# Kernel optimization log

Measured on AMD Instinct MI355X. Metric: run time of the kernel, lower is better.

## Reference

```python
import jax, jax.numpy as jnp
import numpy as np

N = 8192        # nodes
F_IN = 512      # input feature dim
H1 = 256        # args.hidden1
H2 = 64         # args.hidden2
E = 262144      # edges (avg degree 32)


def setup_inputs() -> dict:
    key = jax.random.key(0)
    ks = jax.random.split(key, 7)
    x = jax.random.normal(ks[0], (N, F_IN), dtype=jnp.float32)
    adj_rows = jax.random.randint(ks[1], (E,), 0, N, dtype=jnp.int32)
    adj_cols = jax.random.randint(ks[2], (E,), 0, N, dtype=jnp.int32)
    adj_vals = jax.random.uniform(ks[3], (E,), dtype=jnp.float32)
    # Xavier-uniform init like reset_parameters()
    def xavier(k, fan_in, fan_out):
        lim = jnp.sqrt(6.0 / (fan_in + fan_out))
        return jax.random.uniform(k, (fan_in, fan_out), jnp.float32, -lim, lim)
    W1 = xavier(ks[4], F_IN, H1)
    W2 = xavier(ks[5], H1, H2)
    W3 = xavier(ks[6], H1, H2)
    return {"x": x, "adj_rows": adj_rows, "adj_cols": adj_cols,
            "adj_vals": adj_vals, "W1": W1, "W2": W2, "W3": W3}


def reference(x, adj_rows, adj_cols, adj_vals, W1, W2, W3):
    n = x.shape[0]

    def spmm(support):
        # sparse [N,N] @ dense [N,D]: gather neighbor rows, scale, scatter-add
        return jax.ops.segment_sum(adj_vals[:, None] * support[adj_cols],
                                   adj_rows, num_segments=n)

    # gc1: dropout(no-op, eval) -> x @ W1 -> SpMM -> relu
    h1 = jax.nn.relu(spmm(x @ W1))
    # gc2 / gc3: identity activation
    mu = spmm(h1 @ W2)
    logvar = spmm(h1 @ W3)
    z = mu  # eval-mode reparameterize returns mu
    # InnerProductDecoder with identity act (dropout no-op in eval)
    adj_recon = z @ z.T  # [N, N]
    return adj_recon, z, mu, logvar
```

## Files before the change

kernel.cpp:

```cpp
#include <hip/hip_runtime.h>
#include <hip/hip_bf16.h>

#define N_NODES 8192
#define F_INDIM 512
#define H1DIM   256
#define H2DIM   64

typedef __bf16 bf16x8 __attribute__((ext_vector_type(8)));
typedef float  floatx4 __attribute__((ext_vector_type(4)));

__global__ void count_rows(const int* __restrict__ rows, int* __restrict__ cnt, int e) {
    int i = blockIdx.x * blockDim.x + threadIdx.x;
    if (i < e) atomicAdd(&cnt[rows[i]], 1);
}

__global__ void scan_rows(const int* __restrict__ cnt, int* __restrict__ row_ptr,
                          int* __restrict__ cursor, int n) {
    __shared__ int sums[1024];
    int t = threadIdx.x;
    int base = t * 8;
    int loc[8];
    int s = 0;
#pragma unroll
    for (int i = 0; i < 8; ++i) { loc[i] = cnt[base + i]; s += loc[i]; }
    sums[t] = s;
    __syncthreads();
    for (int off = 1; off < 1024; off <<= 1) {
        int v = (t >= off) ? sums[t - off] : 0;
        __syncthreads();
        sums[t] += v;
        __syncthreads();
    }
    int run = sums[t] - s;
#pragma unroll
    for (int i = 0; i < 8; ++i) {
        row_ptr[base + i] = run;
        cursor[base + i]  = run;
        run += loc[i];
    }
    if (t == 1023) row_ptr[n] = run;
}

__global__ void scatter_edges(const int* __restrict__ rows, const int* __restrict__ cols,
                              const float* __restrict__ vals, int* __restrict__ cursor,
                              int* __restrict__ csr_col, float* __restrict__ csr_val, int e) {
    int i = blockIdx.x * blockDim.x + threadIdx.x;
    if (i < e) {
        int r = rows[i];
        int slot = atomicAdd(&cursor[r], 1);
        csr_col[slot] = cols[i];
        csr_val[slot] = vals[i];
    }
}

__global__ __launch_bounds__(256) void gemm1_f32(const float* __restrict__ A,
                                                 const float* __restrict__ B,
                                                 float* __restrict__ C) {
    constexpr int K = F_INDIM, NN = H1DIM;
    constexpr int BK = 16, LD = 68;
    __shared__ float As[BK][LD];
    __shared__ float Bs[BK][LD];
    const int tid = threadIdx.x;
    const int tx = tid & 15;
    const int ty = tid >> 4;
    const int bm = blockIdx.y * 64;
    const int bn = blockIdx.x * 64;
    float acc[4][4] = {};

    const int arow = tid >> 2, akc = (tid & 3) * 4;
    const int bkk = tid >> 4, bnc = (tid & 15) * 4;

    for (int k0 = 0; k0 < K; k0 += BK) {
        floatx4 av = *(const floatx4*)&A[(size_t)(bm + arow) * K + k0 + akc];
#pragma unroll
        for (int j = 0; j < 4; ++j) As[akc + j][arow] = av[j];
        *(floatx4*)&Bs[bkk][bnc] = *(const floatx4*)&B[(size_t)(k0 + bkk) * NN + bn + bnc];
        __syncthreads();
#pragma unroll
        for (int kk = 0; kk < BK; ++kk) {
            floatx4 a = *(const floatx4*)&As[kk][ty * 4];
            floatx4 b = *(const floatx4*)&Bs[kk][tx * 4];
#pragma unroll
            for (int i = 0; i < 4; ++i)
#pragma unroll
                for (int j = 0; j < 4; ++j) acc[i][j] += a[i] * b[j];
        }
        __syncthreads();
    }
#pragma unroll
    for (int i = 0; i < 4; ++i) {
        floatx4 o = {acc[i][0], acc[i][1], acc[i][2], acc[i][3]};
        *(floatx4*)&C[(size_t)(bm + ty * 4 + i) * NN + bn + tx * 4] = o;
    }
}

__global__ __launch_bounds__(256) void gemm23_f32(const float* __restrict__ A,
                                                  const float* __restrict__ W2,
                                                  const float* __restrict__ W3,
                                                  float* __restrict__ C2,
                                                  float* __restrict__ C3) {
    constexpr int K = H1DIM, NO = H2DIM;
    constexpr int BK = 16, LDA = 68, LDB = 136;
    __shared__ float As[BK][LDA];
    __shared__ float Bs[BK][LDB];
    const int tid = threadIdx.x;
    const int tx = tid & 15;
    const int ty = tid >> 4;
    const int bm = blockIdx.x * 64;
    float acc[4][8] = {};

    const int arow = tid >> 2, akc = (tid & 3) * 4;

    for (int k0 = 0; k0 < K; k0 += BK) {
        floatx4 av = *(const floatx4*)&A[(size_t)(bm + arow) * K + k0 + akc];
#pragma unroll
        for (int j = 0; j < 4; ++j) As[akc + j][arow] = av[j];
#pragma unroll
        for (int v = 0; v < 2; ++v) {
            int idx = tid + v * 256;
            int kk = idx >> 5, nc = (idx & 31) * 4;
            const float* src = (nc < 64) ? &W2[(size_t)(k0 + kk) * NO + nc]
                                         : &W3[(size_t)(k0 + kk) * NO + nc - 64];
            *(floatx4*)&Bs[kk][nc] = *(const floatx4*)src;
        }
        __syncthreads();
#pragma unroll
        for (int kk = 0; kk < BK; ++kk) {
            floatx4 a = *(const floatx4*)&As[kk][ty * 4];
            floatx4 b0 = *(const floatx4*)&Bs[kk][tx * 8];
            floatx4 b1 = *(const floatx4*)&Bs[kk][tx * 8 + 4];
#pragma unroll
            for (int i = 0; i < 4; ++i) {
#pragma unroll
                for (int j = 0; j < 4; ++j) acc[i][j] += a[i] * b0[j];
#pragma unroll
                for (int j = 0; j < 4; ++j) acc[i][j + 4] += a[i] * b1[j];
            }
        }
        __syncthreads();
    }
    const int c0 = tx * 8;
#pragma unroll
    for (int i = 0; i < 4; ++i) {
        floatx4 o0 = {acc[i][0], acc[i][1], acc[i][2], acc[i][3]};
        floatx4 o1 = {acc[i][4], acc[i][5], acc[i][6], acc[i][7]};
        size_t row = bm + ty * 4 + i;
        if (c0 < 64) {
            *(floatx4*)&C2[row * NO + c0] = o0;
            *(floatx4*)&C2[row * NO + c0 + 4] = o1;
        } else {
            *(floatx4*)&C3[row * NO + c0 - 64] = o0;
            *(floatx4*)&C3[row * NO + c0 - 60] = o1;
        }
    }
}

__global__ __launch_bounds__(256) void spmm_h1(const int* __restrict__ row_ptr,
                                               const int* __restrict__ csr_col,
                                               const float* __restrict__ csr_val,
                                               const float* __restrict__ in,
                                               float* __restrict__ out) {
    __shared__ int   s_col[256];
    __shared__ float s_val[256];
    const int r = blockIdx.x;
    const int d = threadIdx.x;
    const int beg = row_ptr[r];
    const int deg = row_ptr[r + 1] - beg;
    float acc = 0.f;
    for (int base = 0; base < deg; base += 256) {
        __syncthreads();
        if (base + d < deg) {
            s_col[d] = csr_col[beg + base + d];
            s_val[d] = csr_val[beg + base + d];
        }
        __syncthreads();
        int m = deg - base; if (m > 256) m = 256;
        int e = 0;
        for (; e + 4 <= m; e += 4) {
            float x0 = in[(size_t)s_col[e]     * H1DIM + d];
            float x1 = in[(size_t)s_col[e + 1] * H1DIM + d];
            float x2 = in[(size_t)s_col[e + 2] * H1DIM + d];
            float x3 = in[(size_t)s_col[e + 3] * H1DIM + d];
            acc += s_val[e] * x0 + s_val[e + 1] * x1 + s_val[e + 2] * x2 + s_val[e + 3] * x3;
        }
        for (; e < m; ++e) acc += s_val[e] * in[(size_t)s_col[e] * H1DIM + d];
    }
    out[(size_t)r * H1DIM + d] = fmaxf(acc, 0.f);
}

__global__ __launch_bounds__(256) void spmm_mu_logvar(const int* __restrict__ row_ptr,
                                                      const int* __restrict__ csr_col,
                                                      const float* __restrict__ csr_val,
                                                      const float* __restrict__ t2,
                                                      const float* __restrict__ t3,
                                                      float* __restrict__ mu,
                                                      float* __restrict__ z,
                                                      float* __restrict__ logvar,
                                                      __hip_bfloat16* __restrict__ zb) {
    __shared__ int   s_col[2][128];
    __shared__ float s_val[2][128];
    __shared__ int   s_deg[2];
    const int tid = threadIdx.x;
    const int half = tid >> 7;
    const int d = tid & 127;
    const int r = blockIdx.x * 2 + half;
    const int beg = row_ptr[r];
    const int deg = row_ptr[r + 1] - beg;
    if (d == 0) s_deg[half] = deg;
    __syncthreads();
    const int trips = (max(s_deg[0], s_deg[1]) + 127) >> 7;
    const float* src = (d < 64) ? t2 : t3;
    const int dd = d & 63;
    float acc = 0.f;
    for (int t = 0; t < trips; ++t) {
        int base = t * 128;
        __syncthreads();
        if (base + d < deg) {
            s_col[half][d] = csr_col[beg + base + d];
            s_val[half][d] = csr_val[beg + base + d];
        }
        __syncthreads();
        int m = deg - base; if (m > 128) m = 128; if (m < 0) m = 0;
        int e = 0;
        for (; e + 4 <= m; e += 4) {
            float x0 = src[(size_t)s_col[half][e]     * H2DIM + dd];
            float x1 = src[(size_t)s_col[half][e + 1] * H2DIM + dd];
            float x2 = src[(size_t)s_col[half][e + 2] * H2DIM + dd];
            float x3 = src[(size_t)s_col[half][e + 3] * H2DIM + dd];
            acc += s_val[half][e] * x0 + s_val[half][e + 1] * x1
                 + s_val[half][e + 2] * x2 + s_val[half][e + 3] * x3;
        }
        for (; e < m; ++e) acc += s_val[half][e] * src[(size_t)s_col[half][e] * H2DIM + dd];
    }
    size_t o = (size_t)r * H2DIM + dd;
    if (d < 64) {
        mu[o] = acc;
        z[o] = acc;
        zb[o] = __float2bfloat16(acc);
    } else {
        logvar[o] = acc;
    }
}

__global__ __launch_bounds__(256) void zzt_mfma(const __hip_bfloat16* __restrict__ z,
                                                float* __restrict__ C) {
    const int tid = threadIdx.x;
    const int lane = tid & 63;
    const int wave = tid >> 6;
    const int wm = wave >> 1, wn = wave & 1;
    const int m0 = blockIdx.y * 128 + wm * 64;
    const int n0 = blockIdx.x * 128 + wn * 64;
    const int r16 = lane & 15;
    const int quad = lane >> 4;

    floatx4 acc[4][4] = {};
    const char* zb = (const char*)z;

#pragma unroll
    for (int h = 0; h < 2; ++h) {
        bf16x8 a[4], b[4];
#pragma unroll
        for (int mt = 0; mt < 4; ++mt)
            a[mt] = *(const bf16x8*)(zb + (m0 + mt * 16 + r16) * 128 + h * 64 + quad * 16);
#pragma unroll
        for (int nt = 0; nt < 4; ++nt)
            b[nt] = *(const bf16x8*)(zb + (n0 + nt * 16 + r16) * 128 + h * 64 + quad * 16);
#pragma unroll
        for (int mt = 0; mt < 4; ++mt)
#pragma unroll
            for (int nt = 0; nt < 4; ++nt)
                acc[mt][nt] = __builtin_amdgcn_mfma_f32_16x16x32_bf16(a[mt], b[nt], acc[mt][nt], 0, 0, 0);
    }

#pragma unroll
    for (int mt = 0; mt < 4; ++mt)
#pragma unroll
        for (int nt = 0; nt < 4; ++nt)
#pragma unroll
            for (int r = 0; r < 4; ++r) {
                int row = m0 + mt * 16 + quad * 4 + r;
                int col = n0 + nt * 16 + r16;
                C[(size_t)row * N_NODES + col] = acc[mt][nt][r];
            }
}

extern "C" void kernel_launch(void* const* d_in, const int* in_sizes, int n_in,
                              void* d_out, int out_size, void* d_ws, size_t ws_size,
                              hipStream_t stream) {
    const float* x        = (const float*)d_in[0];
    const int*   adj_rows = (const int*)d_in[1];
    const int*   adj_cols = (const int*)d_in[2];
    const float* adj_vals = (const float*)d_in[3];
    const float* W1       = (const float*)d_in[4];
    const float* W2       = (const float*)d_in[5];
    const float* W3       = (const float*)d_in[6];
    const int E = in_sizes[1];
    const int n = N_NODES;

    char* ws = (char*)d_ws;
    size_t off = 0;
    auto alloc = [&](size_t bytes) {
        void* p = ws + off;
        off = (off + bytes + 255) & ~(size_t)255;
        return p;
    };
    int*   cnt     = (int*)alloc((size_t)n * 4);
    int*   row_ptr = (int*)alloc((size_t)(n + 1) * 4);
    int*   cursor  = (int*)alloc((size_t)n * 4);
    int*   csr_col = (int*)alloc((size_t)E * 4);
    float* csr_val = (float*)alloc((size_t)E * 4);
    float* support = (float*)alloc((size_t)n * H1DIM * 4);
    float* h1      = (float*)alloc((size_t)n * H1DIM * 4);
    float* t2      = (float*)alloc((size_t)n * H2DIM * 4);
    float* t3      = (float*)alloc((size_t)n * H2DIM * 4);
    __hip_bfloat16* zb = (__hip_bfloat16*)alloc((size_t)n * H2DIM * 2);

    float* out        = (float*)d_out;
    float* adj_recon  = out;
    float* z_out      = out + (size_t)n * n;
    float* mu_out     = z_out + (size_t)n * H2DIM;
    float* logvar_out = mu_out + (size_t)n * H2DIM;

    hipMemsetAsync(cnt, 0, (size_t)n * 4, stream);
    count_rows<<<(E + 255) / 256, 256, 0, stream>>>(adj_rows, cnt, E);
    scan_rows<<<1, 1024, 0, stream>>>(cnt, row_ptr, cursor, n);
    scatter_edges<<<(E + 255) / 256, 256, 0, stream>>>(adj_rows, adj_cols, adj_vals,
                                                       cursor, csr_col, csr_val, E);

    gemm1_f32<<<dim3(H1DIM / 64, n / 64), 256, 0, stream>>>(x, W1, support);
    spmm_h1<<<n, 256, 0, stream>>>(row_ptr, csr_col, csr_val, support, h1);

    gemm23_f32<<<n / 64, 256, 0, stream>>>(h1, W2, W3, t2, t3);
    spmm_mu_logvar<<<n / 2, 256, 0, stream>>>(row_ptr, csr_col, csr_val, t2, t3,
                                              mu_out, z_out, logvar_out, zb);

    zzt_mfma<<<dim3(n / 128, n / 128), 256, 0, stream>>>(zb, adj_recon);
}
```

Measured before the change: 442.5 us.

## Use split-bf16 MFMA GEMMs and vectorized multi-row SpMM kernels

Replaces the FP32 SIMT GEMMs for x@W1 and h1@[W2|W3] with bf16 MFMA kernels. Each operand is split into high and low bf16 parts and three products are summed, so accuracy stays close to fp32. New kernels cast and split x and transpose-cast the weights first, and spmm_h1 now emits h1 directly in split-bf16 form. Both SpMMs are restructured to process two or four rows per block with float2 loads. This adds extra passes over x and 3x MFMA work in exchange for using the matrix cores instead of FP32 FMAs.

```diff
diff --git a/kernel.cpp b/kernel.cpp
--- a/kernel.cpp
+++ b/kernel.cpp
@@ -7,6 +7,8 @@
 #define H2DIM   64
 
 typedef __bf16 bf16x8 __attribute__((ext_vector_type(8)));
+typedef __bf16 bf16x4 __attribute__((ext_vector_type(4)));
+typedef __bf16 bf16x2 __attribute__((ext_vector_type(2)));
 typedef float  floatx4 __attribute__((ext_vector_type(4)));
 
 __global__ void count_rows(const int* __restrict__ rows, int* __restrict__ cnt, int e) {
@@ -53,150 +55,114 @@
     }
 }
 
-__global__ __launch_bounds__(256) void gemm1_f32(const float* __restrict__ A,
-                                                 const float* __restrict__ B,
-                                                 float* __restrict__ C) {
-    constexpr int K = F_INDIM, NN = H1DIM;
-    constexpr int BK = 16, LD = 68;
-    __shared__ float As[BK][LD];
-    __shared__ float Bs[BK][LD];
+__global__ __launch_bounds__(256) void cast_split_x(const float* __restrict__ x,
+                                                    __bf16* __restrict__ xh,
+                                                    __bf16* __restrict__ xl) {
+    int i = (blockIdx.x * 256 + threadIdx.x) * 4;
+    floatx4 v = *(const floatx4*)&x[i];
+    bf16x4 h, l;
+#pragma unroll
+    for (int j = 0; j < 4; ++j) {
+        __bf16 hv = (__bf16)v[j];
+        h[j] = hv;
+        l[j] = (__bf16)(v[j] - (float)hv);
+    }
+    *(bf16x4*)&xh[i] = h;
+    *(bf16x4*)&xl[i] = l;
+}
+
+__global__ void transpose_cast_w(const float* __restrict__ W1, const float* __restrict__ W2,
+                                 const float* __restrict__ W3,
+                                 __bf16* __restrict__ w1th, __bf16* __restrict__ w1tl,
+                                 __bf16* __restrict__ w23th, __bf16* __restrict__ w23tl) {
+    const int z = blockIdx.z;
+    const float* src; __bf16 *oh, *ol; int K, N, rowoff, outld;
+    if (z == 0)      { src = W1; K = 512; N = 256; oh = w1th;  ol = w1tl;  rowoff = 0;  outld = 512; }
+    else if (z == 1) { src = W2; K = 256; N = 64;  oh = w23th; ol = w23tl; rowoff = 0;  outld = 256; }
+    else             { src = W3; K = 256; N = 64;  oh = w23th; ol = w23tl; rowoff = 64; outld = 256; }
+    const int kt = blockIdx.x, nt = blockIdx.y;
+    if (kt * 32 >= K || nt * 32 >= N) return;
+    __shared__ float tile[32][33];
+    const int tx = threadIdx.x, ty = threadIdx.y;
+#pragma unroll
+    for (int j = 0; j < 4; ++j)
+        tile[ty + 8 * j][tx] = src[(size_t)(kt * 32 + ty + 8 * j) * N + nt * 32 + tx];
+    __syncthreads();
+#pragma unroll
+    for (int j = 0; j < 4; ++j) {
+        int n = nt * 32 + ty + 8 * j;
+        int k = kt * 32 + tx;
+        float v = tile[tx][ty + 8 * j];
+        __bf16 h = (__bf16)v;
+        oh[(size_t)(rowoff + n) * outld + k] = h;
+        ol[(size_t)(rowoff + n) * outld + k] = (__bf16)(v - (float)h);
+    }
+}
+
+__global__ __launch_bounds__(256) void gemm1_mfma(const __bf16* __restrict__ xh,
+                                                  const __bf16* __restrict__ xl,
+                                                  const __bf16* __restrict__ bth,
+                                                  const __bf16* __restrict__ btl,
+                                                  float* __restrict__ C) {
+    constexpr int K = F_INDIM, NN = H1DIM, LDSW = 40;
+    __shared__ __bf16 Ah[64 * LDSW], Al[64 * LDSW], Bh[64 * LDSW], Bl[64 * LDSW];
     const int tid = threadIdx.x;
-    const int tx = tid & 15;
-    const int ty = tid >> 4;
-    const int bm = blockIdx.y * 64;
-    const int bn = blockIdx.x * 64;
-    float acc[4][4] = {};
-
-    const int arow = tid >> 2, akc = (tid & 3) * 4;
-    const int bkk = tid >> 4, bnc = (tid & 15) * 4;
-
-    for (int k0 = 0; k0 < K; k0 += BK) {
-        floatx4 av = *(const floatx4*)&A[(size_t)(bm + arow) * K + k0 + akc];
-#pragma unroll
-        for (int j = 0; j < 4; ++j) As[akc + j][arow] = av[j];
-        *(floatx4*)&Bs[bkk][bnc] = *(const floatx4*)&B[(size_t)(k0 + bkk) * NN + bn + bnc];
-        __syncthreads();
-#pragma unroll
-        for (int kk = 0; kk < BK; ++kk) {
-            floatx4 a = *(const floatx4*)&As[kk][ty * 4];
-            floatx4 b = *(const floatx4*)&Bs[kk][tx * 4];
-#pragma unroll
-            for (int i = 0; i < 4; ++i)
-#pragma unroll
-                for (int j = 0; j < 4; ++j) acc[i][j] += a[i] * b[j];
-        }
-        __syncthreads();
-    }
-#pragma unroll
-    for (int i = 0; i < 4; ++i) {
-        floatx4 o = {acc[i][0], acc[i][1], acc[i][2], acc[i][3]};
-        *(floatx4*)&C[(size_t)(bm + ty * 4 + i) * NN + bn + tx * 4] = o;
-    }
-}
-
-__global__ __launch_bounds__(256) void gemm23_f32(const float* __restrict__ A,
-                                                  const float* __restrict__ W2,
-                                                  const float* __restrict__ W3,
-                                                  float* __restrict__ C2,
-                                                  float* __restrict__ C3) {
-    constexpr int K = H1DIM, NO = H2DIM;
-    constexpr int BK = 16, LDA = 68, LDB = 136;
-    __shared__ float As[BK][LDA];
-    __shared__ float Bs[BK][LDB];
-    const int tid = threadIdx.x;
-    const int tx = tid & 15;
-    const int ty = tid >> 4;
-    const int bm = blockIdx.x * 64;
-    float acc[4][8] = {};
-
-    const int arow = tid >> 2, akc = (tid & 3) * 4;
-
-    for (int k0 = 0; k0 < K; k0 += BK) {
-        floatx4 av = *(const floatx4*)&A[(size_t)(bm + arow) * K + k0 + akc];
-#pragma unroll
-        for (int j = 0; j < 4; ++j) As[akc + j][arow] = av[j];
-#pragma unroll
-        for (int v = 0; v < 2; ++v) {
-            int idx = tid + v * 256;
-            int kk = idx >> 5, nc = (idx & 31) * 4;
-            const float* src = (nc < 64) ? &W2[(size_t)(k0 + kk) * NO + nc]
-                                         : &W3[(size_t)(k0 + kk) * NO + nc - 64];
-            *(floatx4*)&Bs[kk][nc] = *(const floatx4*)src;
-        }
-        __syncthreads();
-#pragma unroll
-        for (int kk = 0; kk < BK; ++kk) {
-            floatx4 a = *(const floatx4*)&As[kk][ty * 4];
-            floatx4 b0 = *(const floatx4*)&Bs[kk][tx * 8];
-            floatx4 b1 = *(const floatx4*)&Bs[kk][tx * 8 + 4];
+    const int m0 = blockIdx.y * 64, n0 = blockIdx.x * 64;
+    const int lane = tid & 63, wv = tid >> 6;
+    const int wm = wv >> 1, wn = wv & 1;
+    const int r16 = lane & 15, q = lane >> 4;
+    const int sr = tid >> 2, sc = (tid & 3) * 8;
+    floatx4 acc[2][2] = {};
+
+    for (int k0 = 0; k0 < K; k0 += 32) {
+        bf16x8 va  = *(const bf16x8*)&xh [(size_t)(m0 + sr) * K + k0 + sc];
+        bf16x8 vb  = *(const bf16x8*)&bth[(size_t)(n0 + sr) * K + k0 + sc];
+        bf16x8 va2 = *(const bf16x8*)&xl [(size_t)(m0 + sr) * K + k0 + sc];
+        bf16x8 vb2 = *(const bf16x8*)&btl[(size_t)(n0 + sr) * K + k0 + sc];
+        __syncthreads();
+        *(bf16x8*)&Ah[sr * LDSW + sc] = va;
+        *(bf16x8*)&Bh[sr * LDSW + sc] = vb;
+        *(bf16x8*)&Al[sr * LDSW + sc] = va2;
+        *(bf16x8*)&Bl[sr * LDSW + sc] = vb2;
+        __syncthreads();
+        bf16x8 ah[2], al[2], bh[2], bl[2];
+#pragma unroll
+        for (int mt = 0; mt < 2; ++mt) {
+            ah[mt] = *(const bf16x8*)&Ah[(wm * 32 + mt * 16 + r16) * LDSW + q * 8];
+            al[mt] = *(const bf16x8*)&Al[(wm * 32 + mt * 16 + r16) * LDSW + q * 8];
+        }
+#pragma unroll
+        for (int nt = 0; nt < 2; ++nt) {
+            bh[nt] = *(const bf16x8*)&Bh[(wn * 32 + nt * 16 + r16) * LDSW + q * 8];
+            bl[nt] = *(const bf16x8*)&Bl[(wn * 32 + nt * 16 + r16) * LDSW + q * 8];
+        }
+#pragma unroll
+        for (int mt = 0; mt < 2; ++mt)
+#pragma unroll
+            for (int nt = 0; nt < 2; ++nt) {
+                acc[mt][nt] = __builtin_amdgcn_mfma_f32_16x16x32_bf16(ah[mt], bh[nt], acc[mt][nt], 0, 0, 0);
+                acc[mt][nt] = __builtin_amdgcn_mfma_f32_16x16x32_bf16(ah[mt], bl[nt], acc[mt][nt], 0, 0, 0);
+                acc[mt][nt] = __builtin_amdgcn_mfma_f32_16x16x32_bf16(al[mt], bh[nt], acc[mt][nt], 0, 0, 0);
+            }
+    }
+#pragma unroll
+    for (int mt = 0; mt < 2; ++mt)
+#pragma unroll
+        for (int nt = 0; nt < 2; ++nt)
 #pragma unroll
             for (int i = 0; i < 4; ++i) {
-#pragma unroll
-                for (int j = 0; j < 4; ++j) acc[i][j] += a[i] * b0[j];
-#pragma unroll
-                for (int j = 0; j < 4; ++j) acc[i][j + 4] += a[i] * b1[j];
+                int row = m0 + wm * 32 + mt * 16 + q * 4 + i;
+                int col = n0 + wn * 32 + nt * 16 + r16;
+                C[(size_t)row * NN + col] = acc[mt][nt][i];
             }
-        }
-        __syncthreads();
-    }
-    const int c0 = tx * 8;
-#pragma unroll
-    for (int i = 0; i < 4; ++i) {
-        floatx4 o0 = {acc[i][0], acc[i][1], acc[i][2], acc[i][3]};
-        floatx4 o1 = {acc[i][4], acc[i][5], acc[i][6], acc[i][7]};
-        size_t row = bm + ty * 4 + i;
-        if (c0 < 64) {
-            *(floatx4*)&C2[row * NO + c0] = o0;
-            *(floatx4*)&C2[row * NO + c0 + 4] = o1;
-        } else {
-            *(floatx4*)&C3[row * NO + c0 - 64] = o0;
-            *(floatx4*)&C3[row * NO + c0 - 60] = o1;
-        }
-    }
 }
 
 __global__ __launch_bounds__(256) void spmm_h1(const int* __restrict__ row_ptr,
                                                const int* __restrict__ csr_col,
                                                const float* __restrict__ csr_val,
                                                const float* __restrict__ in,
-                                               float* __restrict__ out) {
-    __shared__ int   s_col[256];
-    __shared__ float s_val[256];
-    const int r = blockIdx.x;
-    const int d = threadIdx.x;
-    const int beg = row_ptr[r];
-    const int deg = row_ptr[r + 1] - beg;
-    float acc = 0.f;
-    for (int base = 0; base < deg; base += 256) {
-        __syncthreads();
-        if (base + d < deg) {
-            s_col[d] = csr_col[beg + base + d];
-            s_val[d] = csr_val[beg + base + d];
-        }
-        __syncthreads();
-        int m = deg - base; if (m > 256) m = 256;
-        int e = 0;
-        for (; e + 4 <= m; e += 4) {
-            float x0 = in[(size_t)s_col[e]     * H1DIM + d];
-            float x1 = in[(size_t)s_col[e + 1] * H1DIM + d];
-            float x2 = in[(size_t)s_col[e + 2] * H1DIM + d];
-            float x3 = in[(size_t)s_col[e + 3] * H1DIM + d];
-            acc += s_val[e] * x0 + s_val[e + 1] * x1 + s_val[e + 2] * x2 + s_val[e + 3] * x3;
-        }
-        for (; e < m; ++e) acc += s_val[e] * in[(size_t)s_col[e] * H1DIM + d];
-    }
-    out[(size_t)r * H1DIM + d] = fmaxf(acc, 0.f);
-}
-
-__global__ __launch_bounds__(256) void spmm_mu_logvar(const int* __restrict__ row_ptr,
-                                                      const int* __restrict__ csr_col,
-                                                      const float* __restrict__ csr_val,
-                                                      const float* __restrict__ t2,
-                                                      const float* __restrict__ t3,
-                                                      float* __restrict__ mu,
-                                                      float* __restrict__ z,
-                                                      float* __restrict__ logvar,
-                                                      __hip_bfloat16* __restrict__ zb) {
+                                               __bf16* __restrict__ h1h,
+                                               __bf16* __restrict__ h1l) {
     __shared__ int   s_col[2][128];
     __shared__ float s_val[2][128];
     __shared__ int   s_deg[2];
@@ -209,9 +175,8 @@
     if (d == 0) s_deg[half] = deg;
     __syncthreads();
     const int trips = (max(s_deg[0], s_deg[1]) + 127) >> 7;
-    const float* src = (d < 64) ? t2 : t3;
-    const int dd = d & 63;
-    float acc = 0.f;
+    const float2* in2 = (const float2*)in;
+    float ax = 0.f, ay = 0.f;
     for (int t = 0; t < trips; ++t) {
         int base = t * 128;
         __syncthreads();
@@ -223,26 +188,171 @@
         int m = deg - base; if (m > 128) m = 128; if (m < 0) m = 0;
         int e = 0;
         for (; e + 4 <= m; e += 4) {
-            float x0 = src[(size_t)s_col[half][e]     * H2DIM + dd];
-            float x1 = src[(size_t)s_col[half][e + 1] * H2DIM + dd];
-            float x2 = src[(size_t)s_col[half][e + 2] * H2DIM + dd];
-            float x3 = src[(size_t)s_col[half][e + 3] * H2DIM + dd];
-            acc += s_val[half][e] * x0 + s_val[half][e + 1] * x1
-                 + s_val[half][e + 2] * x2 + s_val[half][e + 3] * x3;
-        }
-        for (; e < m; ++e) acc += s_val[half][e] * src[(size_t)s_col[half][e] * H2DIM + dd];
-    }
-    size_t o = (size_t)r * H2DIM + dd;
-    if (d < 64) {
-        mu[o] = acc;
-        z[o] = acc;
-        zb[o] = __float2bfloat16(acc);
+            float2 x0 = in2[(size_t)s_col[half][e]     * 128 + d];
+            float2 x1 = in2[(size_t)s_col[half][e + 1] * 128 + d];
+            float2 x2 = in2[(size_t)s_col[half][e + 2] * 128 + d];
+            float2 x3 = in2[(size_t)s_col[half][e + 3] * 128 + d];
+            float v0 = s_val[half][e], v1 = s_val[half][e + 1];
+            float v2 = s_val[half][e + 2], v3 = s_val[half][e + 3];
+            ax += v0 * x0.x + v1 * x1.x + v2 * x2.x + v3 * x3.x;
+            ay += v0 * x0.y + v1 * x1.y + v2 * x2.y + v3 * x3.y;
+        }
+        for (; e < m; ++e) {
+            float2 xv = in2[(size_t)s_col[half][e] * 128 + d];
+            float v = s_val[half][e];
+            ax += v * xv.x;
+            ay += v * xv.y;
+        }
+    }
+    float rx = fmaxf(ax, 0.f), ry = fmaxf(ay, 0.f);
+    __bf16 hx = (__bf16)rx, hy = (__bf16)ry;
+    bf16x2 hv = {hx, hy};
+    bf16x2 lv = {(__bf16)(rx - (float)hx), (__bf16)(ry - (float)hy)};
+    *(bf16x2*)&h1h[(size_t)r * H1DIM + d * 2] = hv;
+    *(bf16x2*)&h1l[(size_t)r * H1DIM + d * 2] = lv;
+}
+
+__global__ __launch_bounds__(256) void gemm23_mfma(const __bf16* __restrict__ ag_h,
+                                                   const __bf16* __restrict__ ag_l,
+                                                   const __bf16* __restrict__ bth,
+                                                   const __bf16* __restrict__ btl,
+                                                   float* __restrict__ t2,
+                                                   float* __restrict__ t3) {
+    constexpr int K = H1DIM, LDSW = 40;
+    __shared__ __bf16 Ah[32 * LDSW], Al[32 * LDSW], Bh[128 * LDSW], Bl[128 * LDSW];
+    const int tid = threadIdx.x;
+    const int m0 = blockIdx.x * 32;
+    const int lane = tid & 63, wn = tid >> 6;
+    const int r16 = lane & 15, q = lane >> 4;
+    const int ta = tid & 127;
+    const int ar = ta >> 2, ac = (ta & 3) * 8;
+    floatx4 acc[2][2] = {};
+
+    for (int k0 = 0; k0 < K; k0 += 32) {
+        const __bf16* asrc = (tid < 128) ? ag_h : ag_l;
+        bf16x8 va = *(const bf16x8*)&asrc[(size_t)(m0 + ar) * K + k0 + ac];
+        bf16x8 vbh[2], vbl[2];
+#pragma unroll
+        for (int v = 0; v < 2; ++v) {
+            int id = tid + v * 256;
+            int br = id >> 2, bc = (id & 3) * 8;
+            vbh[v] = *(const bf16x8*)&bth[(size_t)br * K + k0 + bc];
+            vbl[v] = *(const bf16x8*)&btl[(size_t)br * K + k0 + bc];
+        }
+        __syncthreads();
+        {
+            __bf16* adst = (tid < 128) ? Ah : Al;
+            *(bf16x8*)&adst[ar * LDSW + ac] = va;
+        }
+#pragma unroll
+        for (int v = 0; v < 2; ++v) {
+            int id = tid + v * 256;
+            int br = id >> 2, bc = (id & 3) * 8;
+            *(bf16x8*)&Bh[br * LDSW + bc] = vbh[v];
+            *(bf16x8*)&Bl[br * LDSW + bc] = vbl[v];
+        }
+        __syncthreads();
+        bf16x8 ah[2], al[2], bh[2], bl[2];
+#pragma unroll
+        for (int mt = 0; mt < 2; ++mt) {
+            ah[mt] = *(const bf16x8*)&Ah[(mt * 16 + r16) * LDSW + q * 8];
+            al[mt] = *(const bf16x8*)&Al[(mt * 16 + r16) * LDSW + q * 8];
+        }
+#pragma unroll
+        for (int nt = 0; nt < 2; ++nt) {
+            bh[nt] = *(const bf16x8*)&Bh[(wn * 32 + nt * 16 + r16) * LDSW + q * 8];
+            bl[nt] = *(const bf16x8*)&Bl[(wn * 32 + nt * 16 + r16) * LDSW + q * 8];
+        }
+#pragma unroll
+        for (int mt = 0; mt < 2; ++mt)
+#pragma unroll
+            for (int nt = 0; nt < 2; ++nt) {
+                acc[mt][nt] = __builtin_amdgcn_mfma_f32_16x16x32_bf16(ah[mt], bh[nt], acc[mt][nt], 0, 0, 0);
+                acc[mt][nt] = __builtin_amdgcn_mfma_f32_16x16x32_bf16(ah[mt], bl[nt], acc[mt][nt], 0, 0, 0);
+                acc[mt][nt] = __builtin_amdgcn_mfma_f32_16x16x32_bf16(al[mt], bh[nt], acc[mt][nt], 0, 0, 0);
+            }
+    }
+#pragma unroll
+    for (int mt = 0; mt < 2; ++mt)
+#pragma unroll
+        for (int nt = 0; nt < 2; ++nt)
+#pragma unroll
+            for (int i = 0; i < 4; ++i) {
+                int row = m0 + mt * 16 + q * 4 + i;
+                int col = wn * 32 + nt * 16 + r16;
+                float vv = acc[mt][nt][i];
+                if (col < 64) t2[(size_t)row * H2DIM + col] = vv;
+                else          t3[(size_t)row * H2DIM + col - 64] = vv;
+            }
+}
+
+__global__ __launch_bounds__(256) void spmm_mu_logvar(const int* __restrict__ row_ptr,
+                                                      const int* __restrict__ csr_col,
+                                                      const float* __restrict__ csr_val,
+                                                      const float* __restrict__ t2,
+                                                      const float* __restrict__ t3,
+                                                      float* __restrict__ mu,
+                                                      float* __restrict__ z,
+                                                      float* __restrict__ logvar,
+                                                      __bf16* __restrict__ zb) {
+    __shared__ int   s_col[4][64];
+    __shared__ float s_val[4][64];
+    __shared__ int   s_deg[4];
+    const int tid = threadIdx.x;
+    const int rl = tid >> 6;
+    const int d = tid & 63;
+    const int r = blockIdx.x * 4 + rl;
+    const int beg = row_ptr[r];
+    const int deg = row_ptr[r + 1] - beg;
+    if (d == 0) s_deg[rl] = deg;
+    __syncthreads();
+    const int md = max(max(s_deg[0], s_deg[1]), max(s_deg[2], s_deg[3]));
+    const int trips = (md + 63) >> 6;
+    const float2* src2 = (const float2*)((d < 32) ? t2 : t3);
+    const int dd = d & 31;
+    float ax = 0.f, ay = 0.f;
+    for (int t = 0; t < trips; ++t) {
+        int base = t * 64;
+        __syncthreads();
+        if (base + d < deg) {
+            s_col[rl][d] = csr_col[beg + base + d];
+            s_val[rl][d] = csr_val[beg + base + d];
+        }
+        __syncthreads();
+        int m = deg - base; if (m > 64) m = 64; if (m < 0) m = 0;
+        int e = 0;
+        for (; e + 4 <= m; e += 4) {
+            float2 x0 = src2[(size_t)s_col[rl][e]     * 32 + dd];
+            float2 x1 = src2[(size_t)s_col[rl][e + 1] * 32 + dd];
+            float2 x2 = src2[(size_t)s_col[rl][e + 2] * 32 + dd];
+            float2 x3 = src2[(size_t)s_col[rl][e + 3] * 32 + dd];
+            float v0 = s_val[rl][e], v1 = s_val[rl][e + 1];
+            float v2 = s_val[rl][e + 2], v3 = s_val[rl][e + 3];
+            ax += v0 * x0.x + v1 * x1.x + v2 * x2.x + v3 * x3.x;
+            ay += v0 * x0.y + v1 * x1.y + v2 * x2.y + v3 * x3.y;
+        }
+        for (; e < m; ++e) {
+            float2 xv = src2[(size_t)s_col[rl][e] * 32 + dd];
+            float v = s_val[rl][e];
+            ax += v * xv.x;
+            ay += v * xv.y;
+        }
+    }
+    if (d < 32) {
+        size_t o2 = (size_t)r * 32 + dd;
+        float2 v = {ax, ay};
+        ((float2*)mu)[o2] = v;
+        ((float2*)z)[o2] = v;
+        bf16x2 b = {(__bf16)ax, (__bf16)ay};
+        *(bf16x2*)&zb[o2 * 2] = b;
     } else {
-        logvar[o] = acc;
-    }
-}
-
-__global__ __launch_bounds__(256) void zzt_mfma(const __hip_bfloat16* __restrict__ z,
+        size_t o2 = (size_t)r * 32 + dd;
+        float2 v = {ax, ay};
+        ((float2*)logvar)[o2] = v;
+    }
+}
+
+__global__ __launch_bounds__(256) void zzt_mfma(const __bf16* __restrict__ z,
                                                 float* __restrict__ C) {
     const int tid = threadIdx.x;
     const int lane = tid & 63;
@@ -304,16 +414,23 @@
         off = (off + bytes + 255) & ~(size_t)255;
         return p;
     };
-    int*   cnt     = (int*)alloc((size_t)n * 4);
-    int*   row_ptr = (int*)alloc((size_t)(n + 1) * 4);
-    int*   cursor  = (int*)alloc((size_t)n * 4);
-    int*   csr_col = (int*)alloc((size_t)E * 4);
-    float* csr_val = (float*)alloc((size_t)E * 4);
-    float* support = (float*)alloc((size_t)n * H1DIM * 4);
-    float* h1      = (float*)alloc((size_t)n * H1DIM * 4);
-    float* t2      = (float*)alloc((size_t)n * H2DIM * 4);
-    float* t3      = (float*)alloc((size_t)n * H2DIM * 4);
-    __hip_bfloat16* zb = (__hip_bfloat16*)alloc((size_t)n * H2DIM * 2);
+    int*    cnt     = (int*)alloc((size_t)n * 4);
+    int*    row_ptr = (int*)alloc((size_t)(n + 1) * 4);
+    int*    cursor  = (int*)alloc((size_t)n * 4);
+    int*    csr_col = (int*)alloc((size_t)E * 4);
+    float*  csr_val = (float*)alloc((size_t)E * 4);
+    __bf16* xh      = (__bf16*)alloc((size_t)n * F_INDIM * 2);
+    __bf16* xl      = (__bf16*)alloc((size_t)n * F_INDIM * 2);
+    __bf16* w1th    = (__bf16*)alloc((size_t)H1DIM * F_INDIM * 2);
+    __bf16* w1tl    = (__bf16*)alloc((size_t)H1DIM * F_INDIM * 2);
+    __bf16* w23th   = (__bf16*)alloc((size_t)(2 * H2DIM) * H1DIM * 2);
+    __bf16* w23tl   = (__bf16*)alloc((size_t)(2 * H2DIM) * H1DIM * 2);
+    float*  support = (float*)alloc((size_t)n * H1DIM * 4);
+    __bf16* h1h     = (__bf16*)alloc((size_t)n * H1DIM * 2);
+    __bf16* h1l     = (__bf16*)alloc((size_t)n * H1DIM * 2);
+    float*  t2      = (float*)alloc((size_t)n * H2DIM * 4);
+    float*  t3      = (float*)alloc((size_t)n * H2DIM * 4);
+    __bf16* zb      = (__bf16*)alloc((size_t)n * H2DIM * 2);
 
     float* out        = (float*)d_out;
     float* adj_recon  = out;
@@ -327,11 +444,15 @@
     scatter_edges<<<(E + 255) / 256, 256, 0, stream>>>(adj_rows, adj_cols, adj_vals,
                                                        cursor, csr_col, csr_val, E);
 
-    gemm1_f32<<<dim3(H1DIM / 64, n / 64), 256, 0, stream>>>(x, W1, support);
-    spmm_h1<<<n, 256, 0, stream>>>(row_ptr, csr_col, csr_val, support, h1);
-
-    gemm23_f32<<<n / 64, 256, 0, stream>>>(h1, W2, W3, t2, t3);
-    spmm_mu_logvar<<<n / 2, 256, 0, stream>>>(row_ptr, csr_col, csr_val, t2, t3,
+    cast_split_x<<<(n * F_INDIM) / (256 * 4), 256, 0, stream>>>(x, xh, xl);
+    transpose_cast_w<<<dim3(16, 8, 3), dim3(32, 8), 0, stream>>>(W1, W2, W3,
+                                                                 w1th, w1tl, w23th, w23tl);
+
+    gemm1_mfma<<<dim3(H1DIM / 64, n / 64), 256, 0, stream>>>(xh, xl, w1th, w1tl, support);
+    spmm_h1<<<n / 2, 256, 0, stream>>>(row_ptr, csr_col, csr_val, support, h1h, h1l);
+
+    gemm23_mfma<<<n / 32, 256, 0, stream>>>(h1h, h1l, w23th, w23tl, t2, t3);
+    spmm_mu_logvar<<<n / 4, 256, 0, stream>>>(row_ptr, csr_col, csr_val, t2, t3,
                                               mu_out, z_out, logvar_out, zb);
 
     zzt_mfma<<<dim3(n / 128, n / 128), 256, 0, stream>>>(zb, adj_recon);
```

New measurement: 405.0 us. 1.09x faster.
